# Optimization experiments

Measured on AMD Instinct MI355X. Metric: run time of the kernel, lower is better.

Reference implementation:

```python
import jax, jax.numpy as jnp
import numpy as np

B, S, DIM, SECL = 32, 2048, 1024, 16  # dim = 2*hidden_dim


def setup_inputs() -> dict:
    key = jax.random.key(0)
    ks = jax.random.split(key, 10)
    return {
        "dec_hidden": jax.random.normal(ks[0], (B, DIM), jnp.float32),
        "enc_output": jax.random.normal(ks[1], (B, S, DIM), jnp.float32),
        "enc_feature": jax.random.normal(ks[2], (B, S, DIM), jnp.float32),
        "enc_mask": jnp.ones((B, S), jnp.float32),
        "sec_attn": jax.random.uniform(ks[3], (B, SECL), jnp.float32),
        "coverage": jax.random.uniform(ks[4], (B, S), jnp.float32),
        "W_dec": jax.random.normal(ks[5], (DIM, DIM), jnp.float32) * (1.0 / np.sqrt(DIM)),
        "b_dec": jax.random.normal(ks[6], (DIM,), jnp.float32) * 0.01,
        "v": jax.random.normal(ks[7], (DIM,), jnp.float32) * (1.0 / np.sqrt(DIM)),
        "w_cov": jax.random.normal(ks[8], (DIM,), jnp.float32) * 0.1,
    }


def reference(dec_hidden, enc_output, enc_feature, enc_mask, sec_attn, coverage,
              W_dec, b_dec, v, w_cov):
    # dec_feature: [B, dim], broadcast over src_len
    dec_feature = dec_hidden @ W_dec.T + b_dec
    # att_features = enc_feature + dec_feature + coverage * w_cov  -> [B, S, dim]
    att = enc_feature + dec_feature[:, None, :] + coverage[:, :, None] * w_cov[None, None, :]
    # scalar score per position: v . tanh(att)  -> [B, S]
    score = jnp.einsum('bsd,d->bs', jnp.tanh(att), v)
    # NOTE: the original multiplies sec_attn*score into attn_dist but immediately
    # overwrites it with softmax(score)*mask, so sec_attn does not affect outputs.
    attn = jax.nn.softmax(score, axis=1) * enc_mask
    attn = attn / jnp.sum(attn, axis=1, keepdims=True)
    # context = attn @ enc_output  -> [B, dim]
    context = jnp.einsum('bs,bsd->bd', attn, enc_output)
    coverage_new = coverage + attn
    return context, attn, coverage_new
```

## Files before the change

kernel.cpp:

```cpp
#include <hip/hip_runtime.h>

#define BB 32
#define SS 2048
#define DD 1024

typedef float f32x4 __attribute__((ext_vector_type(4)));

#if defined(__has_builtin)
#  if __has_builtin(__builtin_amdgcn_exp2f)
#    define EXP2F(x) __builtin_amdgcn_exp2f(x)
#  endif
#  if __has_builtin(__builtin_amdgcn_rcpf)
#    define RCPF(x) __builtin_amdgcn_rcpf(x)
#  endif
#endif
#ifndef EXP2F
#  define EXP2F(x) exp2f(x)
#endif
#ifndef RCPF
#  define RCPF(x) (1.0f / (x))
#endif

#define LOG2E 1.44269504088896340736f

__device__ __forceinline__ float fast_tanh(float x) {
    x = fminf(fmaxf(x, -20.0f), 20.0f);
    float e = EXP2F(x * (2.0f * LOG2E));
    return (e - 1.0f) * RCPF(e + 1.0f);
}

__device__ __forceinline__ f32x4 ntload4(const float* p) {
    return __builtin_nontemporal_load((const f32x4*)p);
}

__global__ __launch_bounds__(256) void k_decfeat(
    const float* __restrict__ dh, const float* __restrict__ W,
    const float* __restrict__ bd, float* __restrict__ df,
    float* __restrict__ ctx) {
    if (blockIdx.x < BB) {
        f32x4 z = {0.f, 0.f, 0.f, 0.f};
        ((f32x4*)ctx)[blockIdx.x * 256 + threadIdx.x] = z;
    }
    int wave = threadIdx.x >> 6;
    int lane = threadIdx.x & 63;
    int o = blockIdx.x * 4 + wave;
    int b = o >> 10, i = o & 1023;
    const float4* wrow = (const float4*)(W + (size_t)i * DD);
    const float4* drow = (const float4*)(dh + (size_t)b * DD);
    float acc = 0.0f;
#pragma unroll
    for (int r = 0; r < 4; ++r) {
        float4 w4 = wrow[lane + 64 * r];
        float4 d4 = drow[lane + 64 * r];
        acc += w4.x * d4.x + w4.y * d4.y + w4.z * d4.z + w4.w * d4.w;
    }
#pragma unroll
    for (int off = 32; off; off >>= 1) acc += __shfl_down(acc, off, 64);
    if (lane == 0) df[o] = acc + bd[i];
}

__global__ __launch_bounds__(256) void k_score(
    const float* __restrict__ ef, const float* __restrict__ df,
    const float* __restrict__ cov, const float* __restrict__ v,
    const float* __restrict__ wc, float* __restrict__ E) {
    int b  = blockIdx.x >> 8;
    int s0 = (blockIdx.x & 255) * 8;
    int t  = threadIdx.x;
    float4 v4 = ((const float4*)v)[t];
    float4 w4 = ((const float4*)wc)[t];
    float4 d4 = ((const float4*)(df + (size_t)b * DD))[t];
    float part[8];
#pragma unroll
    for (int k = 0; k < 8; ++k) {
        int s = s0 + k;
        float c = cov[b * SS + s];
        f32x4 e4 = ntload4(ef + ((size_t)b * SS + s) * DD + t * 4);
        float t0 = fast_tanh(e4.x + d4.x + c * w4.x);
        float t1 = fast_tanh(e4.y + d4.y + c * w4.y);
        float t2 = fast_tanh(e4.z + d4.z + c * w4.z);
        float t3 = fast_tanh(e4.w + d4.w + c * w4.w);
        part[k] = v4.x * t0 + v4.y * t1 + v4.z * t2 + v4.w * t3;
    }
    __shared__ float red[4][8];
    int lane = t & 63, wave = t >> 6;
#pragma unroll
    for (int k = 0; k < 8; ++k) {
        float p = part[k];
#pragma unroll
        for (int off = 32; off; off >>= 1) p += __shfl_down(p, off, 64);
        if (lane == 0) red[wave][k] = p;
    }
    __syncthreads();
    if (t < 8) {
        float sc = red[0][t] + red[1][t] + red[2][t] + red[3][t];
        E[b * SS + s0 + t] = EXP2F(sc * LOG2E);
    }
}

__global__ __launch_bounds__(256) void k_ctx_part(
    const float* __restrict__ eo, const float* __restrict__ E,
    const float* __restrict__ mask, const float* __restrict__ cov,
    float* __restrict__ attn, float* __restrict__ covnew,
    float* __restrict__ ctx) {
    int b = blockIdx.x >> 5, ch = blockIdx.x & 31;
    int t = threadIdx.x;
    int lane = t & 63, wave = t >> 6;
    float sum = 0.0f;
#pragma unroll
    for (int k = 0; k < 8; ++k) {
        int s = t + 256 * k;
        sum += E[b * SS + s] * mask[b * SS + s];
    }
#pragma unroll
    for (int off = 32; off; off >>= 1) sum += __shfl_down(sum, off, 64);
    __shared__ float red[4];
    __shared__ float invs;
    if (lane == 0) red[wave] = sum;
    __syncthreads();
    if (t == 0) invs = RCPF(red[0] + red[1] + red[2] + red[3]);
    __syncthreads();
    int s0 = ch * 64;
    __shared__ float als[64];
    if (t < 64) {
        int s = s0 + t;
        float a = E[b * SS + s] * mask[b * SS + s] * invs;
        attn[b * SS + s] = a;
        covnew[b * SS + s] = cov[b * SS + s] + a;
        als[t] = a;
    }
    __syncthreads();
    const float* base = eo + ((size_t)b * SS + s0) * DD;
    f32x4 acc = {0.f, 0.f, 0.f, 0.f};
#pragma unroll 8
    for (int k = 0; k < 64; ++k) {
        f32x4 e4 = ntload4(base + (size_t)k * DD + t * 4);
        acc += als[k] * e4;
    }
    float* cp = ctx + (size_t)b * DD + t * 4;
    atomicAdd(cp + 0, acc.x);
    atomicAdd(cp + 1, acc.y);
    atomicAdd(cp + 2, acc.z);
    atomicAdd(cp + 3, acc.w);
}

extern "C" void kernel_launch(void* const* d_in, const int* in_sizes, int n_in,
                              void* d_out, int out_size, void* d_ws, size_t ws_size,
                              hipStream_t stream) {
    const float* dec_hidden  = (const float*)d_in[0];
    const float* enc_output  = (const float*)d_in[1];
    const float* enc_feature = (const float*)d_in[2];
    const float* enc_mask    = (const float*)d_in[3];
    const float* coverage    = (const float*)d_in[5];
    const float* W_dec       = (const float*)d_in[6];
    const float* b_dec       = (const float*)d_in[7];
    const float* v           = (const float*)d_in[8];
    const float* w_cov       = (const float*)d_in[9];

    float* ctx    = (float*)d_out;
    float* attn   = (float*)d_out + BB * DD;
    float* covnew = (float*)d_out + BB * DD + BB * SS;

    char* ws = (char*)d_ws;
    float* df = (float*)(ws);
    float* E  = (float*)(ws + 131072);

    k_decfeat  <<<8192,  256, 0, stream>>>(dec_hidden, W_dec, b_dec, df, ctx);
    k_score    <<<8192,  256, 0, stream>>>(enc_feature, df, coverage, v, w_cov, E);
    k_ctx_part <<<BB*32, 256, 0, stream>>>(enc_output, E, enc_mask, coverage,
                                           attn, covnew, ctx);
}
```

Before: 100.5 us.

## Restructure decoder-feature GEMV to keep weight rows in registers across batch

The decoder projection kernel now gives each 32-lane group one output row of W and holds that row in registers. It then loops over all 32 batch rows, instead of launching one wave per (batch, row) pair that re-reads W for every batch. This removes the 32x redundant traffic on W and shrinks the grid from 8192 blocks to 128. The cost is much less parallelism: only 128 blocks on a many-CU device, each running a serial batch loop with shuffle reductions.

```diff
diff --git a/kernel.cpp b/kernel.cpp
--- a/kernel.cpp
+++ b/kernel.cpp
@@ -41,22 +41,28 @@
         f32x4 z = {0.f, 0.f, 0.f, 0.f};
         ((f32x4*)ctx)[blockIdx.x * 256 + threadIdx.x] = z;
     }
-    int wave = threadIdx.x >> 6;
-    int lane = threadIdx.x & 63;
-    int o = blockIdx.x * 4 + wave;
-    int b = o >> 10, i = o & 1023;
-    const float4* wrow = (const float4*)(W + (size_t)i * DD);
-    const float4* drow = (const float4*)(dh + (size_t)b * DD);
-    float acc = 0.0f;
+    int t = threadIdx.x;
+    int cg = t >> 5, lane32 = t & 31;
+    int i = blockIdx.x * 8 + cg;
+    const float* wrow = W + (size_t)i * DD;
+    f32x4 w[8];
 #pragma unroll
-    for (int r = 0; r < 4; ++r) {
-        float4 w4 = wrow[lane + 64 * r];
-        float4 d4 = drow[lane + 64 * r];
-        acc += w4.x * d4.x + w4.y * d4.y + w4.z * d4.z + w4.w * d4.w;
+    for (int j = 0; j < 8; ++j)
+        w[j] = *(const f32x4*)(wrow + lane32 * 4 + 128 * j);
+    float bi = bd[i];
+    for (int b = 0; b < BB; ++b) {
+        const float* drow = dh + (size_t)b * DD;
+        f32x4 acc4 = {0.f, 0.f, 0.f, 0.f};
+#pragma unroll
+        for (int j = 0; j < 8; ++j) {
+            f32x4 d = *(const f32x4*)(drow + lane32 * 4 + 128 * j);
+            acc4 += w[j] * d;
+        }
+        float acc = acc4.x + acc4.y + acc4.z + acc4.w;
+#pragma unroll
+        for (int off = 16; off; off >>= 1) acc += __shfl_down(acc, off, 32);
+        if (lane32 == 0) df[(size_t)b * DD + i] = acc + bi;
     }
-#pragma unroll
-    for (int off = 32; off; off >>= 1) acc += __shfl_down(acc, off, 64);
-    if (lane == 0) df[o] = acc + bd[i];
 }
 
 __global__ __launch_bounds__(256) void k_score(
@@ -164,7 +170,7 @@
     float* df = (float*)(ws);
     float* E  = (float*)(ws + 131072);
 
-    k_decfeat  <<<8192,  256, 0, stream>>>(dec_hidden, W_dec, b_dec, df, ctx);
+    k_decfeat  <<<128,   256, 0, stream>>>(dec_hidden, W_dec, b_dec, df, ctx);
     k_score    <<<8192,  256, 0, stream>>>(enc_feature, df, coverage, v, w_cov, E);
     k_ctx_part <<<BB*32, 256, 0, stream>>>(enc_output, E, enc_mask, coverage,
                                            attn, covnew, ctx);
```

Measured after the change: 108.5 us. 8.0% more time.

## Register-tile dec GEMV, enlarge score tiles, precompute masked partial sums

Applied to the files above, without the earlier changes.

The decoder-feature GEMV now has each wave compute a 4x4 block of (output row, batch) pairs. W and dec_hidden loads are reused across 16 accumulators instead of one dot product per wave, cutting redundant W reads. The score kernel processes 16 positions per block, folds the mask into the exponentiated score, and writes per-tile partial sums. This lets the context kernel read 128 partials instead of rescanning 2048 E and mask values in every block. The trade-off is higher register pressure from the 4x4 f32x4 accumulators, fewer blocks for the GEMV and score launches, and an extra workspace array.

```diff
diff --git a/kernel.cpp b/kernel.cpp
--- a/kernel.cpp
+++ b/kernel.cpp
@@ -41,37 +41,56 @@
         f32x4 z = {0.f, 0.f, 0.f, 0.f};
         ((f32x4*)ctx)[blockIdx.x * 256 + threadIdx.x] = z;
     }
-    int wave = threadIdx.x >> 6;
-    int lane = threadIdx.x & 63;
-    int o = blockIdx.x * 4 + wave;
-    int b = o >> 10, i = o & 1023;
-    const float4* wrow = (const float4*)(W + (size_t)i * DD);
-    const float4* drow = (const float4*)(dh + (size_t)b * DD);
-    float acc = 0.0f;
+    int wave = threadIdx.x >> 6, lane = threadIdx.x & 63;
+    int gw = blockIdx.x * 4 + wave;
+    int i0 = (gw >> 3) * 4;
+    int b0 = (gw & 7) * 4;
+    f32x4 acc[4][4];
 #pragma unroll
-    for (int r = 0; r < 4; ++r) {
-        float4 w4 = wrow[lane + 64 * r];
-        float4 d4 = drow[lane + 64 * r];
-        acc += w4.x * d4.x + w4.y * d4.y + w4.z * d4.z + w4.w * d4.w;
+    for (int j = 0; j < 4; ++j)
+#pragma unroll
+        for (int k = 0; k < 4; ++k) acc[j][k] = (f32x4){0.f, 0.f, 0.f, 0.f};
+    for (int c = 0; c < 4; ++c) {
+        int off = c * 256 + lane * 4;
+        f32x4 w4[4], d4[4];
+#pragma unroll
+        for (int j = 0; j < 4; ++j)
+            w4[j] = *(const f32x4*)(W + (size_t)(i0 + j) * DD + off);
+#pragma unroll
+        for (int k = 0; k < 4; ++k)
+            d4[k] = *(const f32x4*)(dh + (size_t)(b0 + k) * DD + off);
+#pragma unroll
+        for (int j = 0; j < 4; ++j)
+#pragma unroll
+            for (int k = 0; k < 4; ++k) acc[j][k] += w4[j] * d4[k];
     }
 #pragma unroll
-    for (int off = 32; off; off >>= 1) acc += __shfl_down(acc, off, 64);
-    if (lane == 0) df[o] = acc + bd[i];
+    for (int j = 0; j < 4; ++j)
+#pragma unroll
+        for (int k = 0; k < 4; ++k) {
+            f32x4 a = acc[j][k];
+            float s = a.x + a.y + a.z + a.w;
+#pragma unroll
+            for (int o = 32; o; o >>= 1) s += __shfl_down(s, o, 64);
+            if (lane == 0) df[(size_t)(b0 + k) * DD + i0 + j] = s + bd[i0 + j];
+        }
 }
 
 __global__ __launch_bounds__(256) void k_score(
     const float* __restrict__ ef, const float* __restrict__ df,
     const float* __restrict__ cov, const float* __restrict__ v,
-    const float* __restrict__ wc, float* __restrict__ E) {
-    int b  = blockIdx.x >> 8;
-    int s0 = (blockIdx.x & 255) * 8;
+    const float* __restrict__ wc, const float* __restrict__ mask,
+    float* __restrict__ EM, float* __restrict__ em_part) {
+    int tile = blockIdx.x & 127;
+    int b  = blockIdx.x >> 7;
+    int s0 = tile * 16;
     int t  = threadIdx.x;
     float4 v4 = ((const float4*)v)[t];
     float4 w4 = ((const float4*)wc)[t];
     float4 d4 = ((const float4*)(df + (size_t)b * DD))[t];
-    float part[8];
+    float part[16];
 #pragma unroll
-    for (int k = 0; k < 8; ++k) {
+    for (int k = 0; k < 16; ++k) {
         int s = s0 + k;
         float c = cov[b * SS + s];
         f32x4 e4 = ntload4(ef + ((size_t)b * SS + s) * DD + t * 4);
@@ -81,36 +100,41 @@
         float t3 = fast_tanh(e4.w + d4.w + c * w4.w);
         part[k] = v4.x * t0 + v4.y * t1 + v4.z * t2 + v4.w * t3;
     }
-    __shared__ float red[4][8];
+    __shared__ float red[4][16];
+    __shared__ float em16[16];
     int lane = t & 63, wave = t >> 6;
 #pragma unroll
-    for (int k = 0; k < 8; ++k) {
+    for (int k = 0; k < 16; ++k) {
         float p = part[k];
 #pragma unroll
         for (int off = 32; off; off >>= 1) p += __shfl_down(p, off, 64);
         if (lane == 0) red[wave][k] = p;
     }
     __syncthreads();
-    if (t < 8) {
+    if (t < 16) {
         float sc = red[0][t] + red[1][t] + red[2][t] + red[3][t];
-        E[b * SS + s0 + t] = EXP2F(sc * LOG2E);
+        float em = EXP2F(sc * LOG2E) * mask[b * SS + s0 + t];
+        EM[b * SS + s0 + t] = em;
+        em16[t] = em;
+    }
+    __syncthreads();
+    if (t == 0) {
+        float s = 0.f;
+#pragma unroll
+        for (int k = 0; k < 16; ++k) s += em16[k];
+        em_part[b * 128 + tile] = s;
     }
 }
 
 __global__ __launch_bounds__(256) void k_ctx_part(
-    const float* __restrict__ eo, const float* __restrict__ E,
-    const float* __restrict__ mask, const float* __restrict__ cov,
+    const float* __restrict__ eo, const float* __restrict__ EM,
+    const float* __restrict__ cov, const float* __restrict__ em_part,
     float* __restrict__ attn, float* __restrict__ covnew,
     float* __restrict__ ctx) {
     int b = blockIdx.x >> 5, ch = blockIdx.x & 31;
     int t = threadIdx.x;
     int lane = t & 63, wave = t >> 6;
-    float sum = 0.0f;
-#pragma unroll
-    for (int k = 0; k < 8; ++k) {
-        int s = t + 256 * k;
-        sum += E[b * SS + s] * mask[b * SS + s];
-    }
+    float sum = (t < 128) ? em_part[b * 128 + t] : 0.0f;
 #pragma unroll
     for (int off = 32; off; off >>= 1) sum += __shfl_down(sum, off, 64);
     __shared__ float red[4];
@@ -123,7 +147,7 @@
     __shared__ float als[64];
     if (t < 64) {
         int s = s0 + t;
-        float a = E[b * SS + s] * mask[b * SS + s] * invs;
+        float a = EM[b * SS + s] * invs;
         attn[b * SS + s] = a;
         covnew[b * SS + s] = cov[b * SS + s] + a;
         als[t] = a;
@@ -161,11 +185,13 @@
     float* covnew = (float*)d_out + BB * DD + BB * SS;
 
     char* ws = (char*)d_ws;
-    float* df = (float*)(ws);
-    float* E  = (float*)(ws + 131072);
+    float* df      = (float*)(ws);
+    float* EM      = (float*)(ws + 131072);
+    float* em_part = (float*)(ws + 393216);
 
-    k_decfeat  <<<8192,  256, 0, stream>>>(dec_hidden, W_dec, b_dec, df, ctx);
-    k_score    <<<8192,  256, 0, stream>>>(enc_feature, df, coverage, v, w_cov, E);
-    k_ctx_part <<<BB*32, 256, 0, stream>>>(enc_output, E, enc_mask, coverage,
-                                           attn, covnew, ctx);
+    k_decfeat  <<<512,   256, 0, stream>>>(dec_hidden, W_dec, b_dec, df, ctx);
+    k_score    <<<4096,  256, 0, stream>>>(enc_feature, df, coverage, v, w_cov,
+                                           enc_mask, EM, em_part);
+    k_ctx_part <<<BB*32, 256, 0, stream>>>(enc_output, EM, coverage,
+                                           em_part, attn, covnew, ctx);
 }
```

Measured after the change: 102.3 us. Within noise of the previous version (+1.8%).

## Fuse score and context kernels with deferred softmax normalization

Applied to the files above, without the earlier changes.

The score computation and the context accumulation now run in one kernel. Each block computes unnormalized exp scores for its 64 positions, writes them and a partial sum, then accumulates the context from enc_output using those weights. A small finalize kernel adds up the partial sums and rescales attn, coverage and ctx. This removes the separate score pass and its launch, plus the redundant full-row sum each context block used to recompute. The cost is a much smaller grid (1024 blocks instead of 8192) for the enc_feature pass, with eight serialized sub-steps separated by barriers.

```diff
diff --git a/kernel.cpp b/kernel.cpp
--- a/kernel.cpp
+++ b/kernel.cpp
@@ -59,76 +59,57 @@
     if (lane == 0) df[o] = acc + bd[i];
 }
 
-__global__ __launch_bounds__(256) void k_score(
+__global__ __launch_bounds__(256) void k_fused(
     const float* __restrict__ ef, const float* __restrict__ df,
     const float* __restrict__ cov, const float* __restrict__ v,
-    const float* __restrict__ wc, float* __restrict__ E) {
-    int b  = blockIdx.x >> 8;
-    int s0 = (blockIdx.x & 255) * 8;
-    int t  = threadIdx.x;
+    const float* __restrict__ wc, const float* __restrict__ mask,
+    const float* __restrict__ eo, float* __restrict__ attn_un,
+    float* __restrict__ sum_part, float* __restrict__ ctx) {
+    int b = blockIdx.x >> 5, ch = blockIdx.x & 31;
+    int s0 = ch * 64;
+    int t = threadIdx.x;
+    int lane = t & 63, wave = t >> 6;
     float4 v4 = ((const float4*)v)[t];
     float4 w4 = ((const float4*)wc)[t];
     float4 d4 = ((const float4*)(df + (size_t)b * DD))[t];
-    float part[8];
+    __shared__ float als[64];
+    __shared__ float red[4][8];
+    for (int sub = 0; sub < 8; ++sub) {
+        int ss0 = s0 + sub * 8;
+        float part[8];
 #pragma unroll
-    for (int k = 0; k < 8; ++k) {
-        int s = s0 + k;
-        float c = cov[b * SS + s];
-        f32x4 e4 = ntload4(ef + ((size_t)b * SS + s) * DD + t * 4);
-        float t0 = fast_tanh(e4.x + d4.x + c * w4.x);
-        float t1 = fast_tanh(e4.y + d4.y + c * w4.y);
-        float t2 = fast_tanh(e4.z + d4.z + c * w4.z);
-        float t3 = fast_tanh(e4.w + d4.w + c * w4.w);
-        part[k] = v4.x * t0 + v4.y * t1 + v4.z * t2 + v4.w * t3;
+        for (int k = 0; k < 8; ++k) {
+            int s = ss0 + k;
+            float c = cov[b * SS + s];
+            f32x4 e4 = ntload4(ef + ((size_t)b * SS + s) * DD + t * 4);
+            float t0 = fast_tanh(e4.x + d4.x + c * w4.x);
+            float t1 = fast_tanh(e4.y + d4.y + c * w4.y);
+            float t2 = fast_tanh(e4.z + d4.z + c * w4.z);
+            float t3 = fast_tanh(e4.w + d4.w + c * w4.w);
+            part[k] = v4.x * t0 + v4.y * t1 + v4.z * t2 + v4.w * t3;
+        }
+#pragma unroll
+        for (int k = 0; k < 8; ++k) {
+            float p = part[k];
+#pragma unroll
+            for (int off = 32; off; off >>= 1) p += __shfl_down(p, off, 64);
+            if (lane == 0) red[wave][k] = p;
+        }
+        __syncthreads();
+        if (t < 8) {
+            float sc = red[0][t] + red[1][t] + red[2][t] + red[3][t];
+            float em = EXP2F(sc * LOG2E) * mask[b * SS + ss0 + t];
+            attn_un[b * SS + ss0 + t] = em;
+            als[sub * 8 + t] = em;
+        }
+        __syncthreads();
     }
-    __shared__ float red[4][8];
-    int lane = t & 63, wave = t >> 6;
+    if (t < 64) {
+        float s = als[t];
 #pragma unroll
-    for (int k = 0; k < 8; ++k) {
-        float p = part[k];
-#pragma unroll
-        for (int off = 32; off; off >>= 1) p += __shfl_down(p, off, 64);
-        if (lane == 0) red[wave][k] = p;
+        for (int off = 32; off; off >>= 1) s += __shfl_down(s, off, 64);
+        if (t == 0) sum_part[b * 32 + ch] = s;
     }
-    __syncthreads();
-    if (t < 8) {
-        float sc = red[0][t] + red[1][t] + red[2][t] + red[3][t];
-        E[b * SS + s0 + t] = EXP2F(sc * LOG2E);
-    }
-}
-
-__global__ __launch_bounds__(256) void k_ctx_part(
-    const float* __restrict__ eo, const float* __restrict__ E,
-    const float* __restrict__ mask, const float* __restrict__ cov,
-    float* __restrict__ attn, float* __restrict__ covnew,
-    float* __restrict__ ctx) {
-    int b = blockIdx.x >> 5, ch = blockIdx.x & 31;
-    int t = threadIdx.x;
-    int lane = t & 63, wave = t >> 6;
-    float sum = 0.0f;
-#pragma unroll
-    for (int k = 0; k < 8; ++k) {
-        int s = t + 256 * k;
-        sum += E[b * SS + s] * mask[b * SS + s];
-    }
-#pragma unroll
-    for (int off = 32; off; off >>= 1) sum += __shfl_down(sum, off, 64);
-    __shared__ float red[4];
-    __shared__ float invs;
-    if (lane == 0) red[wave] = sum;
-    __syncthreads();
-    if (t == 0) invs = RCPF(red[0] + red[1] + red[2] + red[3]);
-    __syncthreads();
-    int s0 = ch * 64;
-    __shared__ float als[64];
-    if (t < 64) {
-        int s = s0 + t;
-        float a = E[b * SS + s] * mask[b * SS + s] * invs;
-        attn[b * SS + s] = a;
-        covnew[b * SS + s] = cov[b * SS + s] + a;
-        als[t] = a;
-    }
-    __syncthreads();
     const float* base = eo + ((size_t)b * SS + s0) * DD;
     f32x4 acc = {0.f, 0.f, 0.f, 0.f};
 #pragma unroll 8
@@ -141,6 +122,31 @@
     atomicAdd(cp + 1, acc.y);
     atomicAdd(cp + 2, acc.z);
     atomicAdd(cp + 3, acc.w);
+}
+
+__global__ __launch_bounds__(256) void k_finalize(
+    const float* __restrict__ sum_part, const float* __restrict__ cov,
+    float* __restrict__ attn, float* __restrict__ covnew,
+    float* __restrict__ ctx) {
+    int b = blockIdx.x >> 3, dt = blockIdx.x & 7;
+    int t = threadIdx.x;
+    __shared__ float invs;
+    if (t < 32) {
+        float s = sum_part[b * 32 + t];
+#pragma unroll
+        for (int off = 16; off; off >>= 1) s += __shfl_down(s, off, 32);
+        if (t == 0) invs = RCPF(s);
+    }
+    __syncthreads();
+    float inv = invs;
+    int s = dt * 256 + t;
+    float a = attn[b * SS + s] * inv;
+    attn[b * SS + s] = a;
+    covnew[b * SS + s] = cov[b * SS + s] + a;
+    if (t < 128) {
+        int d = dt * 128 + t;
+        ctx[(size_t)b * DD + d] *= inv;
+    }
 }
 
 extern "C" void kernel_launch(void* const* d_in, const int* in_sizes, int n_in,
@@ -161,11 +167,11 @@
     float* covnew = (float*)d_out + BB * DD + BB * SS;
 
     char* ws = (char*)d_ws;
-    float* df = (float*)(ws);
-    float* E  = (float*)(ws + 131072);
+    float* df       = (float*)(ws);
+    float* sum_part = (float*)(ws + 131072);
 
     k_decfeat  <<<8192,  256, 0, stream>>>(dec_hidden, W_dec, b_dec, df, ctx);
-    k_score    <<<8192,  256, 0, stream>>>(enc_feature, df, coverage, v, w_cov, E);
-    k_ctx_part <<<BB*32, 256, 0, stream>>>(enc_output, E, enc_mask, coverage,
-                                           attn, covnew, ctx);
+    k_fused    <<<BB*32, 256, 0, stream>>>(enc_feature, df, coverage, v, w_cov,
+                                           enc_mask, enc_output, attn, sum_part, ctx);
+    k_finalize <<<BB*8,  256, 0, stream>>>(sum_part, coverage, attn, covnew, ctx);
 }
```

New measurement: 97.66 us. 2.8% less time.
